# Kernel optimization log

Measured on AMD Instinct MI355X. Metric: run time of the kernel, lower is better.

Reference implementation:

```python
import jax, jax.numpy as jnp
import numpy as np
from jax import lax

B, H, W, C = 4, 32, 32, 256
N_HEADS = 8
HEAD_D = C // N_HEADS  # 32


def position_encoding(height, width, channels):
    # Faithful to Position_Embedding: for size=256, dim=128; both even/odd use sin.
    dim = channels // 2
    y_embed = np.repeat(np.arange(1, height + 1), width).reshape(height, width)
    x_embed = np.broadcast_to(np.arange(1, width + 1), (height, width))
    div_term = 10000.0 ** (2 * (np.arange(dim) // 2) / dim)
    pos_x = x_embed[:, :, None] / div_term
    pos_y = y_embed[:, :, None] / div_term
    px = np.concatenate((np.sin(pos_x[:, :, 0::2]), np.sin(pos_x[:, :, 1::2])), axis=2)
    py = np.concatenate((np.sin(pos_y[:, :, 0::2]), np.sin(pos_y[:, :, 1::2])), axis=2)
    pe = np.concatenate((py, px), axis=2)[None].astype(np.float32)  # [1,H,W,C]
    return jnp.asarray(pe)


def setup_inputs() -> dict:
    key = jax.random.key(0)
    ks = jax.random.split(key, 10)
    s = 0.02  # weight init scale
    return {
        "src1": jax.random.normal(ks[0], (B, H, W, C), jnp.float32),
        "src2": jax.random.normal(ks[1], (B, H, W, C), jnp.float32),
        "Wq1": jax.random.normal(ks[2], (C, C), jnp.float32) * s,
        "bq1": jnp.zeros((C,), jnp.float32),
        "Wq2": jax.random.normal(ks[3], (C, C), jnp.float32) * s,
        "bq2": jnp.zeros((C,), jnp.float32),
        "Wk": jax.random.normal(ks[4], (C, C), jnp.float32) * s,
        "bk": jnp.zeros((C,), jnp.float32),
        "Wv": jax.random.normal(ks[5], (C, C), jnp.float32) * s,
        "bv": jnp.zeros((C,), jnp.float32),
        "conv_w": jax.random.normal(ks[6], (3, 3, 2 * HEAD_D, 2 * HEAD_D), jnp.float32) * s,
        "conv_b": jnp.zeros((2 * HEAD_D,), jnp.float32),
        "Wo": jax.random.normal(ks[7], (C, C), jnp.float32) * s,
        "bo": jnp.zeros((C,), jnp.float32),
    }


def reference(src1, src2, Wq1, bq1, Wq2, bq2, Wk, bk, Wv, bv, conv_w, conv_b, Wo, bo):
    d = HEAD_D
    N = H * W
    pe = position_encoding(H, W, C)  # [1,H,W,C]
    kin = src1 + pe
    q1_in = src1 + pe
    v_in = src1 + pe
    q2_in = src2 + pe

    q1 = q1_in @ Wq1 + bq1  # [B,H,W,C]
    q2 = q2_in @ Wq2 + bq2
    k = kin @ Wk + bk
    v = v_in @ Wv + bv

    # Q head split: 8 heads -> add first 4 and last 4 -> 4 effective heads
    Q1 = q1.reshape(B, N, 8, d)
    q_s_1 = Q1[:, :, :4, :] + Q1[:, :, 4:, :]  # [B,N,4,d]
    Q2 = q2.reshape(B, N, 8, d)
    q_s_2 = Q2[:, :, :4, :] + Q2[:, :, 4:, :]  # [B,N,4,d]

    # K split: self path (first 4d channels), co path (conv on 2d, concat last 2d)
    k_s = k[..., : 4 * d]  # [B,H,W,4d]
    k_co_1 = k[..., 4 * d : 6 * d]  # [B,H,W,2d]
    k_co_2 = k[..., 6 * d :]  # [B,H,W,2d]
    k_conv_r = lax.conv_general_dilated(
        k_co_1, conv_w, window_strides=(1, 1), padding="SAME",
        dimension_numbers=("NHWC", "HWIO", "NHWC")) + conv_b
    k_conv = jnp.concatenate([k_conv_r, k_co_2], axis=-1)  # [B,H,W,4d]

    k_s_1 = k_s.reshape(B, N, 4, d)
    k_s_2 = k_conv.reshape(B, N, 4, d)
    v_co = v.reshape(B, N, 8, d).transpose(0, 2, 1, 3)  # [B,8,N,d]

    scale = jnp.sqrt(jnp.float32(d))
    logits_self = jnp.einsum("bnhd,bmhd->bhnm", q_s_1, k_s_1) / scale  # [B,4,N,N]
    logits_co = jnp.einsum("bnhd,bmhd->bhnm", q_s_2, k_s_2) / scale  # [B,4,N,N]
    scaled = jnp.concatenate([logits_co, logits_self], axis=1)  # [B,8,N,N]

    attn = jax.nn.softmax(scaled, axis=-1)
    out = jnp.einsum("bhnm,bhmd->bnhd", attn, v_co).reshape(B, N, C)
    return out @ Wo + bo  # [B,N,C]
```

## Files before the change

### kernel.cpp

```cpp
#include <hip/hip_runtime.h>
#include <cstdint>
#include <cstddef>

typedef __attribute__((ext_vector_type(8))) short short8v;
typedef __attribute__((ext_vector_type(4))) short short4v;
typedef __attribute__((ext_vector_type(4))) float f32x4;
typedef unsigned short ushort_t;

__device__ inline unsigned short f2bf(float x) {
    unsigned int u = __float_as_uint(x);
    return (unsigned short)((u + 0x7FFFu + ((u >> 16) & 1u)) >> 16);
}

__global__ __launch_bounds__(256) void pe_prep_kernel(
    const float* __restrict__ src1, const float* __restrict__ src2,
    const float* __restrict__ Wq1, const float* __restrict__ Wq2,
    const float* __restrict__ Wk, const float* __restrict__ Wv,
    const float* __restrict__ Wo, const float* __restrict__ cw,
    const float* __restrict__ bq1, const float* __restrict__ bq2,
    const float* __restrict__ bk, const float* __restrict__ bv,
    ushort_t* __restrict__ X1, ushort_t* __restrict__ X2,
    ushort_t* __restrict__ WcatT, ushort_t* __restrict__ WoT,
    float* __restrict__ bcat, ushort_t* __restrict__ Wcv2)
{
    __shared__ ushort_t Ts[64][72];
    int bx = blockIdx.x;
    int t = threadIdx.x;

    if (bx < 1024) {
        int n = bx, c = t;
        int row = n >> 5, col = n & 31;
        float pos = (c < 128) ? (float)(row + 1) : (float)(col + 1);
        float freq = expf(-0.14391156831212787f * (float)(c & 63));
        float pe = sinf(pos * freq);
        for (int b = 0; b < 4; ++b) {
            size_t idx = ((size_t)b * 1024 + n) * 256 + c;
            X1[idx] = f2bf(src1[idx] + pe);
            X2[idx] = f2bf(src2[idx] + pe);
        }
        return;
    }

    if (bx < 1088) {
        int idx = bx - 1024;
        int kt = idx & 3, ct = idx >> 2;
        int k0 = kt * 64;
        const float* W; int csrc; int fold = 0; ushort_t* dst; int dstbase;
        if (ct < 2)       { W = Wq1; csrc = ct * 64;        fold = 1; dst = WcatT; dstbase = ct * 64; }
        else if (ct < 4)  { W = Wq2; csrc = (ct - 2) * 64;  fold = 1; dst = WcatT; dstbase = ct * 64; }
        else if (ct < 8)  { W = Wk;  csrc = (ct - 4) * 64;            dst = WcatT; dstbase = ct * 64; }
        else if (ct < 12) { W = Wv;  csrc = (ct - 8) * 64;            dst = WcatT; dstbase = ct * 64; }
        else              { W = Wo;  csrc = (ct - 12) * 64;           dst = WoT;   dstbase = (ct - 12) * 64; }
        if (kt == 0) {
            if (ct == 0 && t < 128) bcat[t] = bq1[t] + bq1[t + 128];
            if (ct == 2 && t < 128) bcat[128 + t] = bq2[t] + bq2[t + 128];
            if (ct == 4) bcat[256 + t] = bk[t];
            if (ct == 8) bcat[512 + t] = bv[t];
        }

        int kr = t >> 2, cq = t & 3;
        #pragma unroll
        for (int i = 0; i < 4; ++i) {
            int cc = cq * 16 + i * 4;
            float4 v = *(const float4*)&W[(size_t)(k0 + kr) * 256 + csrc + cc];
            if (fold) {
                float4 v2 = *(const float4*)&W[(size_t)(k0 + kr) * 256 + csrc + cc + 128];
                v.x += v2.x; v.y += v2.y; v.z += v2.z; v.w += v2.w;
            }
            Ts[kr][cc + 0] = f2bf(v.x); Ts[kr][cc + 1] = f2bf(v.y);
            Ts[kr][cc + 2] = f2bf(v.z); Ts[kr][cc + 3] = f2bf(v.w);
        }
        __syncthreads();
        int cr = t >> 2, kq = t & 3;
        ushort_t tmp[16];
        #pragma unroll
        for (int i = 0; i < 16; ++i) tmp[i] = Ts[kq * 16 + i][cr];
        *(short8v*)&dst[(size_t)(dstbase + cr) * 256 + k0 + kq * 16]     = *(short8v*)&tmp[0];
        *(short8v*)&dst[(size_t)(dstbase + cr) * 256 + k0 + kq * 16 + 8] = *(short8v*)&tmp[8];
        return;
    }

    {
        int tap = bx - 1088;
        int ci = t >> 2, co0 = (t & 3) * 16;
        #pragma unroll
        for (int i = 0; i < 16; ++i)
            Ts[ci][co0 + i] = f2bf(cw[((size_t)(tap * 64 + ci)) * 64 + co0 + i]);
        __syncthreads();
        int co = t >> 2, ci0 = (t & 3) * 16;
        ushort_t tmp[16];
        #pragma unroll
        for (int i = 0; i < 16; ++i) tmp[i] = Ts[ci0 + i][co];
        int kh = ci0 >> 5;
        int f = (tap * 2 + kh) * 4 + (co >> 4);
        int off = f * 512 + (co & 15) * 32 + (ci0 & 31);
        *(short8v*)&Wcv2[off]     = *(short8v*)&tmp[0];
        *(short8v*)&Wcv2[off + 8] = *(short8v*)&tmp[8];
    }
}

__global__ __launch_bounds__(256) void proj_gemm(
    const ushort_t* __restrict__ X1, const ushort_t* __restrict__ X2,
    const ushort_t* __restrict__ WcatT, const float* __restrict__ bcat,
    ushort_t* __restrict__ Qbf, ushort_t* __restrict__ Kbf,
    ushort_t* __restrict__ VTbf, ushort_t* __restrict__ CVbf)
{
    __shared__ ushort_t As[64][136];
    __shared__ ushort_t Bs[64][136];
    int colBase = blockIdx.x * 64, rowBase = blockIdx.y * 64;
    const ushort_t* A = (colBase >= 128 && colBase < 256) ? X2 : X1;
    int tid = threadIdx.x;
    int w = tid >> 6, l = tid & 63, lr = l & 15, g = l >> 4;
    int wr = w >> 1, wc = w & 1;
    int tr = tid >> 2, tq = tid & 3;
    f32x4 acc[2][2] = {};

    for (int kb = 0; kb < 256; kb += 128) {
        #pragma unroll
        for (int i = 0; i < 4; ++i)
            *(short8v*)&As[tr][tq * 32 + i * 8] =
                *(const short8v*)&A[(size_t)(rowBase + tr) * 256 + kb + tq * 32 + i * 8];
        #pragma unroll
        for (int i = 0; i < 4; ++i)
            *(short8v*)&Bs[tr][tq * 32 + i * 8] =
                *(const short8v*)&WcatT[(size_t)(colBase + tr) * 256 + kb + tq * 32 + i * 8];
        __syncthreads();
        #pragma unroll
        for (int ks = 0; ks < 4; ++ks) {
            short8v a0 = *(const short8v*)&As[wr * 32 + lr][ks * 32 + g * 8];
            short8v a1 = *(const short8v*)&As[wr * 32 + 16 + lr][ks * 32 + g * 8];
            short8v b0 = *(const short8v*)&Bs[wc * 32 + lr][ks * 32 + g * 8];
            short8v b1 = *(const short8v*)&Bs[wc * 32 + 16 + lr][ks * 32 + g * 8];
            acc[0][0] = __builtin_amdgcn_mfma_f32_16x16x32_bf16(a0, b0, acc[0][0], 0, 0, 0);
            acc[0][1] = __builtin_amdgcn_mfma_f32_16x16x32_bf16(a0, b1, acc[0][1], 0, 0, 0);
            acc[1][0] = __builtin_amdgcn_mfma_f32_16x16x32_bf16(a1, b0, acc[1][0], 0, 0, 0);
            acc[1][1] = __builtin_amdgcn_mfma_f32_16x16x32_bf16(a1, b1, acc[1][1], 0, 0, 0);
        }
        __syncthreads();
    }

    const float scale = 0.25503532182457352f;
    #pragma unroll
    for (int fr = 0; fr < 2; ++fr)
        #pragma unroll
        for (int fc = 0; fc < 2; ++fc) {
            int c = colBase + wc * 32 + fc * 16 + lr;
            float bv = bcat[c];
            int nb = rowBase + wr * 32 + fr * 16 + g * 4;
            int b = nb >> 10;
            if (c < 512) {
                #pragma unroll
                for (int r = 0; r < 4; ++r) {
                    int n = nb + r;
                    float v = acc[fr][fc][r] + bv;
                    if (c < 128) {
                        int h = 4 + (c >> 5), d = c & 31;
                        Qbf[(((size_t)(b * 8 + h) << 10) | (n & 1023)) * 32 + d] = f2bf(v * scale);
                    } else if (c < 256) {
                        int c2 = c - 128;
                        int h = c2 >> 5, d = c2 & 31;
                        Qbf[(((size_t)(b * 8 + h) << 10) | (n & 1023)) * 32 + d] = f2bf(v * scale);
                    } else {
                        int c3 = c - 256;
                        if (c3 < 128) {
                            int h = 4 + (c3 >> 5), d = c3 & 31;
                            Kbf[(((size_t)(b * 8 + h) << 10) | (n & 1023)) * 32 + d] = f2bf(v);
                        } else if (c3 < 192) {
                            CVbf[(size_t)n * 64 + (c3 - 128)] = f2bf(v);
                        } else {
                            int h = 2 + ((c3 - 192) >> 5), d = c3 & 31;
                            Kbf[(((size_t)(b * 8 + h) << 10) | (n & 1023)) * 32 + d] = f2bf(v);
                        }
                    }
                }
            } else {
                int c4 = c - 512;
                int h = c4 >> 5, d = c4 & 31;
                short4v pk;
                #pragma unroll
                for (int r = 0; r < 4; ++r) pk[r] = (short)f2bf(acc[fr][fc][r] + bv);
                *(short4v*)&VTbf[((size_t)((b * 8 + h) * 32 + d)) * 1024 + (nb & 1023)] = pk;
            }
        }
}

__global__ __launch_bounds__(256) void conv_mfma(
    const ushort_t* __restrict__ CVbf, const ushort_t* __restrict__ Wcv2,
    const float* __restrict__ cb, ushort_t* __restrict__ Kbf)
{
    __shared__ ushort_t Xs[8704];
    int blk = blockIdx.x;
    int b = blk >> 4, y0 = (blk & 15) * 2;
    int tid = threadIdx.x, w = tid >> 6, l = tid & 63, lr = l & 15, g = l >> 4;

    for (int p = tid >> 1; p < 136; p += 128) {
        int ry = p / 34, xc = p % 34;
        int ci0 = (tid & 1) * 32;
        int gy = y0 - 1 + ry, gx = xc - 1;
        int base = p << 6;
        int sw = (xc & 7) << 3;
        if ((unsigned)gy < 32u && (unsigned)gx < 32u) {
            const ushort_t* src = &CVbf[((size_t)(b * 1024 + gy * 32 + gx)) * 64 + ci0];
            #pragma unroll
            for (int k = 0; k < 4; ++k)
                *(short8v*)&Xs[(base + ci0 + k * 8) ^ sw] = *(const short8v*)&src[k * 8];
        } else {
            short8v z = {};
            #pragma unroll
            for (int k = 0; k < 4; ++k)
                *(short8v*)&Xs[(base + ci0 + k * 8) ^ sw] = z;
        }
    }
    __syncthreads();

    int yl = w >> 1, xb = (w & 1) * 16;
    f32x4 acc[4] = {};
    #pragma unroll
    for (int ky = 0; ky < 3; ++ky)
        #pragma unroll
        for (int kx = 0; kx < 3; ++kx) {
            int tap = ky * 3 + kx;
            #pragma unroll
            for (int kh = 0; kh < 2; ++kh) {
                int xa = xb + lr + kx;
                int e = (((yl + ky) * 34 + xa) << 6) + kh * 32 + g * 8;
                short8v af = *(const short8v*)&Xs[e ^ ((xa & 7) << 3)];
                int fb = (tap * 2 + kh) * 4 * 512 + lr * 32 + g * 8;
                #pragma unroll
                for (int nf = 0; nf < 4; ++nf) {
                    short8v bf_ = *(const short8v*)&Wcv2[fb + nf * 512];
                    acc[nf] = __builtin_amdgcn_mfma_f32_16x16x32_bf16(af, bf_, acc[nf], 0, 0, 0);
                }
            }
        }

    #pragma unroll
    for (int nf = 0; nf < 4; ++nf) {
        int co = nf * 16 + lr;
        float bias = cb[co];
        int h = co >> 5, d = co & 31;
        #pragma unroll
        for (int r = 0; r < 4; ++r) {
            int px = w * 16 + g * 4 + r;
            int n = y0 * 32 + px;
            Kbf[(((size_t)(b * 8 + h) << 10) | n) * 32 + d] = f2bf(acc[nf][r] + bias);
        }
    }
}

__global__ __launch_bounds__(256) void attn_mfma3(
    const ushort_t* __restrict__ Qbf, const ushort_t* __restrict__ Kbf,
    const ushort_t* __restrict__ VTbf,
    float* __restrict__ Opart, float* __restrict__ Lpart)
{
    __shared__ ushort_t Kt[64][32];
    __shared__ ushort_t VT[32][72];
    __shared__ ushort_t Ps[4][16][72];

    int bh = blockIdx.y, q0 = blockIdx.x * 64, s = blockIdx.z;
    int tid = threadIdx.x, w = tid >> 6, l = tid & 63, lr = l & 15, g = l >> 4;

    short8v qfrag = *(const short8v*)&Qbf[((size_t)bh * 1024 + q0 + w * 16 + lr) * 32 + g * 8];

    f32x4 accO[2] = {};
    float lsum = 0.f;
    const f32x4 zero = {};

    for (int mt = s * 8; mt < s * 8 + 8; ++mt) {
        int m0 = mt * 64;
        ((short8v*)&Kt[0][0])[tid] =
            *(const short8v*)&Kbf[((size_t)bh * 1024 + m0) * 32 + tid * 8];
        *(short8v*)&VT[tid >> 3][(tid & 7) * 8] =
            *(const short8v*)&VTbf[((size_t)bh * 32 + (tid >> 3)) * 1024 + m0 + (tid & 7) * 8];
        __syncthreads();

        f32x4 st[4];
        #pragma unroll
        for (int t = 0; t < 4; ++t) {
            short8v kf = *(const short8v*)&Kt[t * 16 + lr][g * 8];
            st[t] = __builtin_amdgcn_mfma_f32_16x16x32_bf16(kf, qfrag, zero, 0, 0, 0);
        }

        #pragma unroll
        for (int t = 0; t < 4; ++t) {
            float p0 = exp2f(st[t][0]), p1 = exp2f(st[t][1]);
            float p2 = exp2f(st[t][2]), p3 = exp2f(st[t][3]);
            lsum += (p0 + p1) + (p2 + p3);
            short4v pw;
            pw[0] = (short)f2bf(p0); pw[1] = (short)f2bf(p1);
            pw[2] = (short)f2bf(p2); pw[3] = (short)f2bf(p3);
            *(short4v*)&Ps[w][lr][t * 16 + g * 4] = pw;
        }

        #pragma unroll
        for (int kt = 0; kt < 2; ++kt) {
            short8v pa = *(const short8v*)&Ps[w][lr][kt * 32 + g * 8];
            #pragma unroll
            for (int nt = 0; nt < 2; ++nt) {
                short8v vb = *(const short8v*)&VT[nt * 16 + lr][kt * 32 + g * 8];
                accO[nt] = __builtin_amdgcn_mfma_f32_16x16x32_bf16(pa, vb, accO[nt], 0, 0, 0);
            }
        }
        __syncthreads();
    }

    lsum += __shfl_xor(lsum, 16);
    lsum += __shfl_xor(lsum, 32);
    if (l < 16)
        Lpart[(size_t)(s * 32 + bh) * 1024 + q0 + w * 16 + lr] = lsum;

    #pragma unroll
    for (int nt = 0; nt < 2; ++nt)
        #pragma unroll
        for (int r = 0; r < 4; ++r) {
            int n = q0 + w * 16 + g * 4 + r;
            Opart[((size_t)(s * 32 + bh) * 1024 + n) * 32 + nt * 16 + lr] = accO[nt][r];
        }
}

__global__ __launch_bounds__(256) void attn_merge(
    const float* __restrict__ Opart, const float* __restrict__ Lpart,
    ushort_t* __restrict__ AObf)
{
    int row = blockIdx.x * 32 + (threadIdx.x >> 3);
    int d0 = (threadIdx.x & 7) * 4;
    const size_t SSTR = (size_t)32 * 1024 * 32;
    float4 o0 = *(const float4*)&Opart[(size_t)row * 32 + d0];
    float4 o1 = *(const float4*)&Opart[SSTR + (size_t)row * 32 + d0];
    float inv = 1.0f / (Lpart[row] + Lpart[32768 + row]);
    int bh = row >> 10, n = row & 1023, b = bh >> 3, h = bh & 7;
    short4v pk;
    pk[0] = (short)f2bf((o0.x + o1.x) * inv);
    pk[1] = (short)f2bf((o0.y + o1.y) * inv);
    pk[2] = (short)f2bf((o0.z + o1.z) * inv);
    pk[3] = (short)f2bf((o0.w + o1.w) * inv);
    *(short4v*)&AObf[((size_t)(b * 1024 + n)) * 256 + h * 32 + d0] = pk;
}

__global__ __launch_bounds__(256) void out_gemm(
    const ushort_t* __restrict__ A, const ushort_t* __restrict__ WoT,
    const float* __restrict__ bo, float* __restrict__ out)
{
    __shared__ ushort_t As[64][136];
    __shared__ ushort_t Bs[64][136];
    int colBase = blockIdx.x * 64, rowBase = blockIdx.y * 64;
    int tid = threadIdx.x;
    int w = tid >> 6, l = tid & 63, lr = l & 15, g = l >> 4;
    int wr = w >> 1, wc = w & 1;
    int tr = tid >> 2, tq = tid & 3;
    f32x4 acc[2][2] = {};

    for (int kb = 0; kb < 256; kb += 128) {
        #pragma unroll
        for (int i = 0; i < 4; ++i)
            *(short8v*)&As[tr][tq * 32 + i * 8] =
                *(const short8v*)&A[(size_t)(rowBase + tr) * 256 + kb + tq * 32 + i * 8];
        #pragma unroll
        for (int i = 0; i < 4; ++i)
            *(short8v*)&Bs[tr][tq * 32 + i * 8] =
                *(const short8v*)&WoT[(size_t)(colBase + tr) * 256 + kb + tq * 32 + i * 8];
        __syncthreads();
        #pragma unroll
        for (int ks = 0; ks < 4; ++ks) {
            short8v a0 = *(const short8v*)&As[wr * 32 + lr][ks * 32 + g * 8];
            short8v a1 = *(const short8v*)&As[wr * 32 + 16 + lr][ks * 32 + g * 8];
            short8v b0 = *(const short8v*)&Bs[wc * 32 + lr][ks * 32 + g * 8];
            short8v b1 = *(const short8v*)&Bs[wc * 32 + 16 + lr][ks * 32 + g * 8];
            acc[0][0] = __builtin_amdgcn_mfma_f32_16x16x32_bf16(a0, b0, acc[0][0], 0, 0, 0);
            acc[0][1] = __builtin_amdgcn_mfma_f32_16x16x32_bf16(a0, b1, acc[0][1], 0, 0, 0);
            acc[1][0] = __builtin_amdgcn_mfma_f32_16x16x32_bf16(a1, b0, acc[1][0], 0, 0, 0);
            acc[1][1] = __builtin_amdgcn_mfma_f32_16x16x32_bf16(a1, b1, acc[1][1], 0, 0, 0);
        }
        __syncthreads();
    }

    #pragma unroll
    for (int fr = 0; fr < 2; ++fr)
        #pragma unroll
        for (int fc = 0; fc < 2; ++fc) {
            int c = colBase + wc * 32 + fc * 16 + lr;
            float bv = bo[c];
            int nb = rowBase + wr * 32 + fr * 16 + g * 4;
            #pragma unroll
            for (int r = 0; r < 4; ++r)
                out[(size_t)(nb + r) * 256 + c] = acc[fr][fc][r] + bv;
        }
}

extern "C" void kernel_launch(void* const* d_in, const int* in_sizes, int n_in,
                              void* d_out, int out_size, void* d_ws, size_t ws_size,
                              hipStream_t stream)
{
    const float* src1 = (const float*)d_in[0];
    const float* src2 = (const float*)d_in[1];
    const float* Wq1  = (const float*)d_in[2];
    const float* bq1  = (const float*)d_in[3];
    const float* Wq2  = (const float*)d_in[4];
    const float* bq2  = (const float*)d_in[5];
    const float* Wk   = (const float*)d_in[6];
    const float* bk   = (const float*)d_in[7];
    const float* Wv   = (const float*)d_in[8];
    const float* bv   = (const float*)d_in[9];
    const float* cw   = (const float*)d_in[10];
    const float* cb   = (const float*)d_in[11];
    const float* Wo   = (const float*)d_in[12];
    const float* bo   = (const float*)d_in[13];
    float* out = (float*)d_out;

    char* base = (char*)d_ws;
    const size_t MB = 1u << 20;
    const size_t KB = 1u << 10;
    ushort_t* X1bf = (ushort_t*)(base + 0 * MB);
    ushort_t* X2bf = (ushort_t*)(base + 2 * MB);
    ushort_t* Qbf  = (ushort_t*)(base + 4 * MB);
    ushort_t* Kbf  = (ushort_t*)(base + 6 * MB);
    ushort_t* VTbf = (ushort_t*)(base + 8 * MB);
    ushort_t* AObf = (ushort_t*)(base + 10 * MB);
    ushort_t* CVbf = (ushort_t*)(base + 12 * MB);
    ushort_t* WcatT= (ushort_t*)(base + 12 * MB + 512 * KB);
    ushort_t* WoT  = (ushort_t*)(base + 12 * MB + 896 * KB);
    float*    bcat = (float*)(base + 13 * MB);
    ushort_t* Wcv2 = (ushort_t*)(base + 13 * MB + 4 * KB);
    float*    Opart= (float*)(base + 14 * MB);
    float*    Lpart= (float*)(base + 22 * MB);

    pe_prep_kernel<<<1097, 256, 0, stream>>>(
        src1, src2, Wq1, Wq2, Wk, Wv, Wo, cw, bq1, bq2, bk, bv,
        X1bf, X2bf, WcatT, WoT, bcat, Wcv2);
    proj_gemm<<<dim3(12, 64), 256, 0, stream>>>(
        X1bf, X2bf, WcatT, bcat, Qbf, Kbf, VTbf, CVbf);
    conv_mfma<<<64, 256, 0, stream>>>(CVbf, Wcv2, cb, Kbf);
    attn_mfma3<<<dim3(16, 32, 2), 256, 0, stream>>>(Qbf, Kbf, VTbf, Opart, Lpart);
    attn_merge<<<1024, 256, 0, stream>>>(Opart, Lpart, AObf);
    out_gemm<<<dim3(4, 64), 256, 0, stream>>>(AObf, WoT, bo, out);
}
```

Before: 52.41 us.

## Drop split-KV attention, double-buffer K/V tiles and fuse merge into attention kernel

```diff
diff --git a/kernel.cpp b/kernel.cpp
--- a/kernel.cpp
+++ b/kernel.cpp
@@ -248,17 +248,17 @@
     }
 }
 
-__global__ __launch_bounds__(256) void attn_mfma3(
+__global__ __launch_bounds__(256) void attn_mfma4(
     const ushort_t* __restrict__ Qbf, const ushort_t* __restrict__ Kbf,
-    const ushort_t* __restrict__ VTbf,
-    float* __restrict__ Opart, float* __restrict__ Lpart)
-{
-    __shared__ ushort_t Kt[64][32];
-    __shared__ ushort_t VT[32][72];
+    const ushort_t* __restrict__ VTbf, ushort_t* __restrict__ AObf)
+{
+    __shared__ ushort_t Kt[2][64][32];
+    __shared__ ushort_t VT[2][32][72];
     __shared__ ushort_t Ps[4][16][72];
 
-    int bh = blockIdx.y, q0 = blockIdx.x * 64, s = blockIdx.z;
+    int bh = blockIdx.y, q0 = blockIdx.x * 64;
     int tid = threadIdx.x, w = tid >> 6, l = tid & 63, lr = l & 15, g = l >> 4;
+    int vd = tid >> 3, vn = (tid & 7) * 8;
 
     short8v qfrag = *(const short8v*)&Qbf[((size_t)bh * 1024 + q0 + w * 16 + lr) * 32 + g * 8];
 
@@ -266,18 +266,27 @@
     float lsum = 0.f;
     const f32x4 zero = {};
 
-    for (int mt = s * 8; mt < s * 8 + 8; ++mt) {
-        int m0 = mt * 64;
-        ((short8v*)&Kt[0][0])[tid] =
-            *(const short8v*)&Kbf[((size_t)bh * 1024 + m0) * 32 + tid * 8];
-        *(short8v*)&VT[tid >> 3][(tid & 7) * 8] =
-            *(const short8v*)&VTbf[((size_t)bh * 32 + (tid >> 3)) * 1024 + m0 + (tid & 7) * 8];
-        __syncthreads();
+    ((short8v*)&Kt[0][0][0])[tid] =
+        *(const short8v*)&Kbf[((size_t)bh * 1024) * 32 + tid * 8];
+    *(short8v*)&VT[0][vd][vn] =
+        *(const short8v*)&VTbf[((size_t)bh * 32 + vd) * 1024 + vn];
+
+    for (int mt = 0; mt < 16; ++mt) {
+        int cur = mt & 1, nb = cur ^ 1;
+        __syncthreads();
+
+        short8v kreg, vreg;
+        bool hasNext = (mt + 1) < 16;
+        if (hasNext) {
+            int m1 = (mt + 1) * 64;
+            kreg = *(const short8v*)&Kbf[((size_t)bh * 1024 + m1) * 32 + tid * 8];
+            vreg = *(const short8v*)&VTbf[((size_t)bh * 32 + vd) * 1024 + m1 + vn];
+        }
 
         f32x4 st[4];
         #pragma unroll
         for (int t = 0; t < 4; ++t) {
-            short8v kf = *(const short8v*)&Kt[t * 16 + lr][g * 8];
+            short8v kf = *(const short8v*)&Kt[cur][t * 16 + lr][g * 8];
             st[t] = __builtin_amdgcn_mfma_f32_16x16x32_bf16(kf, qfrag, zero, 0, 0, 0);
         }
 
@@ -297,44 +306,32 @@
             short8v pa = *(const short8v*)&Ps[w][lr][kt * 32 + g * 8];
             #pragma unroll
             for (int nt = 0; nt < 2; ++nt) {
-                short8v vb = *(const short8v*)&VT[nt * 16 + lr][kt * 32 + g * 8];
+                short8v vb = *(const short8v*)&VT[cur][nt * 16 + lr][kt * 32 + g * 8];
                 accO[nt] = __builtin_amdgcn_mfma_f32_16x16x32_bf16(pa, vb, accO[nt], 0, 0, 0);
             }
         }
-        __syncthreads();
+
+        if (hasNext) {
+            ((short8v*)&Kt[nb][0][0])[tid] = kreg;
+            *(short8v*)&VT[nb][vd][vn] = vreg;
+        }
     }
 
     lsum += __shfl_xor(lsum, 16);
     lsum += __shfl_xor(lsum, 32);
-    if (l < 16)
-        Lpart[(size_t)(s * 32 + bh) * 1024 + q0 + w * 16 + lr] = lsum;
-
+
+    int b = bh >> 3, h = bh & 7;
     #pragma unroll
-    for (int nt = 0; nt < 2; ++nt)
-        #pragma unroll
-        for (int r = 0; r < 4; ++r) {
-            int n = q0 + w * 16 + g * 4 + r;
-            Opart[((size_t)(s * 32 + bh) * 1024 + n) * 32 + nt * 16 + lr] = accO[nt][r];
-        }
-}
-
-__global__ __launch_bounds__(256) void attn_merge(
-    const float* __restrict__ Opart, const float* __restrict__ Lpart,
-    ushort_t* __restrict__ AObf)
-{
-    int row = blockIdx.x * 32 + (threadIdx.x >> 3);
-    int d0 = (threadIdx.x & 7) * 4;
-    const size_t SSTR = (size_t)32 * 1024 * 32;
-    float4 o0 = *(const float4*)&Opart[(size_t)row * 32 + d0];
-    float4 o1 = *(const float4*)&Opart[SSTR + (size_t)row * 32 + d0];
-    float inv = 1.0f / (Lpart[row] + Lpart[32768 + row]);
-    int bh = row >> 10, n = row & 1023, b = bh >> 3, h = bh & 7;
-    short4v pk;
-    pk[0] = (short)f2bf((o0.x + o1.x) * inv);
-    pk[1] = (short)f2bf((o0.y + o1.y) * inv);
-    pk[2] = (short)f2bf((o0.z + o1.z) * inv);
-    pk[3] = (short)f2bf((o0.w + o1.w) * inv);
-    *(short4v*)&AObf[((size_t)(b * 1024 + n)) * 256 + h * 32 + d0] = pk;
+    for (int r = 0; r < 4; ++r) {
+        float lv = __uint_as_float((unsigned)__builtin_amdgcn_ds_bpermute(
+            (g * 4 + r) * 4, (int)__float_as_uint(lsum)));
+        float inv = 1.0f / lv;
+        int n = q0 + w * 16 + g * 4 + r;
+        #pragma unroll
+        for (int nt = 0; nt < 2; ++nt)
+            AObf[((size_t)(b * 1024 + n)) * 256 + h * 32 + nt * 16 + lr] =
+                f2bf(accO[nt][r] * inv);
+    }
 }
 
 __global__ __launch_bounds__(256) void out_gemm(
@@ -421,8 +418,6 @@
     ushort_t* WoT  = (ushort_t*)(base + 12 * MB + 896 * KB);
     float*    bcat = (float*)(base + 13 * MB);
     ushort_t* Wcv2 = (ushort_t*)(base + 13 * MB + 4 * KB);
-    float*    Opart= (float*)(base + 14 * MB);
-    float*    Lpart= (float*)(base + 22 * MB);
 
     pe_prep_kernel<<<1097, 256, 0, stream>>>(
         src1, src2, Wq1, Wq2, Wk, Wv, Wo, cw, bq1, bq2, bk, bv,
@@ -430,7 +425,6 @@
     proj_gemm<<<dim3(12, 64), 256, 0, stream>>>(
         X1bf, X2bf, WcatT, bcat, Qbf, Kbf, VTbf, CVbf);
     conv_mfma<<<64, 256, 0, stream>>>(CVbf, Wcv2, cb, Kbf);
-    attn_mfma3<<<dim3(16, 32, 2), 256, 0, stream>>>(Qbf, Kbf, VTbf, Opart, Lpart);
-    attn_merge<<<1024, 256, 0, stream>>>(Opart, Lpart, AObf);
+    attn_mfma4<<<dim3(16, 32), 256, 0, stream>>>(Qbf, Kbf, VTbf, AObf);
     out_gemm<<<dim3(4, 64), 256, 0, stream>>>(AObf, WoT, bo, out);
 }
```

Result: faster. 48.69 us (-7.1%).
